# Optimization experiments

Measured on AMD Instinct MI355X. Metric: run time of the kernel, lower is better.

The kernel has to match this reference:

```python
import jax, jax.numpy as jnp
import numpy as np

B, T = 64, 2048
ENC_DIM, ATT_DIM, RNN_DIM, N_FILT, KSIZE, WIN = 512, 128, 1024, 32, 31, 32


def setup_inputs() -> dict:
    key = jax.random.key(0)
    ks = jax.random.split(key, 10)
    return {
        "attention_hidden_state": jax.random.normal(ks[0], (B, RNN_DIM), jnp.float32),
        "memory": jax.random.normal(ks[1], (B, T, ENC_DIM), jnp.float32),
        "processed_memory": jax.random.normal(ks[2], (B, T, ATT_DIM), jnp.float32),
        "attention_weights_cat": jax.random.uniform(ks[3], (B, 2, T), jnp.float32),
        "mask": jnp.zeros((B, T), jnp.bool_),
        "memory_lengths": jax.random.randint(ks[4], (B,), 0, T, jnp.int32),
        "current_pos": jax.random.uniform(ks[5], (B,), jnp.float32),
        "loc_conv_w": jax.random.normal(ks[6], (N_FILT, 2, KSIZE), jnp.float32) * 0.1,
        "loc_dense_w": jax.random.normal(ks[7], (ATT_DIM, N_FILT), jnp.float32) * 0.1,
        "query_w": jax.random.normal(ks[8], (ATT_DIM, RNN_DIM), jnp.float32) * 0.03,
        "v_w": jax.random.normal(ks[9], (1, ATT_DIM), jnp.float32) * 0.1,
        "pos_offset": jnp.zeros((1,), jnp.float32),
    }


def reference(attention_hidden_state, memory, processed_memory, attention_weights_cat,
              mask, memory_lengths, current_pos,
              loc_conv_w, loc_dense_w, query_w, v_w, pos_offset):
    Bn, Tn, _ = memory.shape
    pad = (KSIZE - 1) // 2
    # location conv: [B,2,T] -> [B,n_filters,T]
    conv = jax.lax.conv_general_dilated(
        attention_weights_cat, loc_conv_w, window_strides=(1,),
        padding=[(pad, pad)], dimension_numbers=("NCH", "OIH", "NCH"))
    # location dense + query projection + processed memory (fused add)
    processed = (jnp.einsum("bft,af->bta", conv, loc_dense_w)
                 + (attention_hidden_state @ query_w.T)[:, None, :]
                 + processed_memory)                      # [B,T,att_dim]
    alignment = jnp.tanh(processed) @ v_w[0]              # [B,T]
    # dynamic windowed mask around current_pos
    cp = current_pos + pos_offset[0]
    max_end = (memory_lengths - 1 - WIN).astype(cp.dtype)
    cp = jnp.minimum(jnp.maximum(cp, jnp.float32(WIN)), max_end)
    mask_start = jnp.round(jnp.maximum(cp - WIN, 0.0))
    mask_end = mask_start + 2 * WIN
    pos = jnp.arange(Tn, dtype=cp.dtype)
    pos_mask = (pos[None, :] >= mask_start[:, None]) & (pos[None, :] <= mask_end[:, None])
    full_mask = mask | ~pos_mask
    alignment = jnp.where(full_mask, jnp.float32(-1e9), alignment)
    attention_weights = jax.nn.softmax(alignment, axis=1)  # [B,T]
    attention_context = jnp.einsum("bt,btd->bd", attention_weights, memory)  # [B,enc_dim]
    new_pos = attention_weights @ jnp.arange(Tn, dtype=attention_weights.dtype)  # [B]
    return attention_context, attention_weights, new_pos
```

## Files before the change

### kernel.cpp

```cpp
#include <hip/hip_runtime.h>
#include <math.h>

#define Bn 64
#define Tn 2048
#define ENC 512
#define ATT 128
#define RNN 1024
#define NF 32
#define KS 31
#define WINR 32
#define WSZ 65
#define HALO 95
#define NTH 512

__global__ __launch_bounds__(NTH)
void attn_fused(
    const float* __restrict__ hidden,
    const float* __restrict__ memory,
    const float* __restrict__ pmem,
    const float* __restrict__ cat,
    const unsigned char* __restrict__ mask,
    const int*  __restrict__ mlen,
    const float* __restrict__ cpos,
    const float* __restrict__ convw,
    const float* __restrict__ densew,
    const float* __restrict__ qw,
    const float* __restrict__ vw,
    const float* __restrict__ posoff,
    float* __restrict__ out)
{
    __shared__ float s_hidden[RNN];
    __shared__ float s_part[NTH];
    __shared__ float s_qproj[ATT];
    __shared__ float s_ldw[ATT * 33];
    __shared__ float s_cw[NF * 2 * KS];
    __shared__ float s_cat[2 * HALO];
    __shared__ float s_conv[WSZ * NF];
    __shared__ float s_pm[WSZ * ATT];
    __shared__ unsigned char s_mk[WSZ];
    __shared__ float s_align[WSZ];
    __shared__ float s_w[WSZ];
    __shared__ float2 s_red[2 * (ENC / 2)];

    const int b = blockIdx.x;
    const int tid = threadIdx.x;

    float cp = cpos[b] + posoff[0];
    float mend = (float)(mlen[b] - 1 - WINR);
    cp = fminf(fmaxf(cp, (float)WINR), mend);
    int s = (int)rintf(fmaxf(cp - (float)WINR, 0.0f));
    if (s < 0) s = 0;
    if (s > Tn - WSZ) s = Tn - WSZ;

    for (int i = tid; i < RNN / 4; i += NTH)
        ((float4*)s_hidden)[i] = ((const float4*)(hidden + (size_t)b * RNN))[i];
    {
        const float4* pmw = (const float4*)(pmem + ((size_t)b * Tn + s) * ATT);
        for (int i = tid; i < WSZ * ATT / 4; i += NTH)
            ((float4*)s_pm)[i] = pmw[i];
    }
    for (int i = tid; i < ATT * NF; i += NTH) {
        int a = i >> 5, f = i & 31;
        s_ldw[a * 33 + f] = densew[i];
    }
    for (int i = tid; i < NF * 2 * KS; i += NTH) s_cw[i] = convw[i];
    for (int i = tid; i < 2 * HALO; i += NTH) {
        int cch = i / HALO, j = i - cch * HALO;
        int t = s - (KS - 1) / 2 + j;
        float v = 0.0f;
        if (t >= 0 && t < Tn) v = cat[((size_t)b * 2 + cch) * Tn + t];
        s_cat[cch * HALO + j] = v;
    }
    if (tid < WSZ) s_mk[tid] = mask[(size_t)b * Tn + s + tid];

    const int c = tid & 255;
    const int g = tid >> 8;
    float2 v[33];
    const float2* m2 = (const float2*)(memory + (size_t)b * Tn * ENC)
                       + (size_t)(s + g) * (ENC / 2) + c;
#pragma unroll
    for (int i = 0; i < 33; i++) {
        int j = g + 2 * i;
        if (j < WSZ) v[i] = m2[(size_t)(2 * i) * (ENC / 2)];
    }
    __syncthreads();

    {
        int a = tid & 127, q = tid >> 7;
        const float4* q4 = (const float4*)(qw + (size_t)a * RNN + q * 256);
        const float4* h4 = (const float4*)(s_hidden + q * 256);
        float acc = 0.0f;
#pragma unroll 8
        for (int i = 0; i < 64; i++) {
            float4 x = q4[i], h = h4[i];
            acc += x.x * h.x + x.y * h.y + x.z * h.z + x.w * h.w;
        }
        s_part[tid] = acc;
    }
    __syncthreads();
    if (tid < ATT)
        s_qproj[tid] = s_part[tid] + s_part[tid + 128] + s_part[tid + 256] + s_part[tid + 384];

    for (int i = tid; i < WSZ * NF; i += NTH) {
        int j = i >> 5, f = i & 31;
        const float* w0 = s_cw + f * 2 * KS;
        const float* c0 = s_cat + j;
        const float* c1 = s_cat + HALO + j;
        float acc = 0.0f;
#pragma unroll
        for (int k = 0; k < KS; k++) acc += c0[k] * w0[k] + c1[k] * w0[KS + k];
        s_conv[i] = acc;
    }
    __syncthreads();

    const int lane = tid & 63;
    const int wv = tid >> 6;
    const float va0 = vw[lane];
    const float va1 = vw[lane + 64];
    for (int j = wv; j < WSZ; j += 8) {
        const float* pmr = s_pm + j * ATT;
        const float* cv = s_conv + j * NF;
        const float* l0 = s_ldw + lane * 33;
        const float* l1 = s_ldw + (lane + 64) * 33;
        float x0 = s_qproj[lane] + pmr[lane];
        float x1 = s_qproj[lane + 64] + pmr[lane + 64];
#pragma unroll
        for (int f = 0; f < NF; f++) {
            float cc = cv[f];
            x0 += cc * l0[f];
            x1 += cc * l1[f];
        }
        float val = tanhf(x0) * va0 + tanhf(x1) * va1;
        for (int off = 32; off > 0; off >>= 1) val += __shfl_down(val, off);
        if (lane == 0) s_align[j] = s_mk[j] ? -1e9f : val;
    }
    __syncthreads();

    if (tid < WSZ) {
        float m = -1e30f;
        for (int j = 0; j < WSZ; j++) m = fmaxf(m, s_align[j]);
        float sum = 0.0f;
        for (int j = 0; j < WSZ; j++) sum += expf(s_align[j] - m);
        s_w[tid] = expf(s_align[tid] - m) / sum;
    }
    __syncthreads();

    if (tid == 0) {
        float np = 0.0f;
        for (int j = 0; j < WSZ; j++) np += s_w[j] * (float)(s + j);
        out[(size_t)Bn * ENC + (size_t)Bn * Tn + b] = np;
    }

    {
        float4* wout = (float4*)(out + (size_t)Bn * ENC + (size_t)b * Tn);
        for (int i = tid; i < Tn / 4; i += NTH) {
            float4 vv;
            float* vp = (float*)&vv;
#pragma unroll
            for (int q = 0; q < 4; q++) {
                int j = i * 4 + q - s;
                vp[q] = (j >= 0 && j < WSZ) ? s_w[j] : 0.0f;
            }
            wout[i] = vv;
        }
    }

    {
        float2 acc = make_float2(0.0f, 0.0f);
#pragma unroll
        for (int i = 0; i < 33; i++) {
            int j = g + 2 * i;
            if (j < WSZ) {
                float wj = s_w[j];
                acc.x += wj * v[i].x;
                acc.y += wj * v[i].y;
            }
        }
        s_red[g * (ENC / 2) + c] = acc;
    }
    __syncthreads();
    if (tid < ENC / 2) {
        float2 a = s_red[tid], bb = s_red[(ENC / 2) + tid];
        float2 r = make_float2(a.x + bb.x, a.y + bb.y);
        ((float2*)out)[(size_t)b * (ENC / 2) + tid] = r;
    }
}

extern "C" void kernel_launch(void* const* d_in, const int* in_sizes, int n_in,
                              void* d_out, int out_size, void* d_ws, size_t ws_size,
                              hipStream_t stream) {
    attn_fused<<<Bn, NTH, 0, stream>>>(
        (const float*)d_in[0],
        (const float*)d_in[1],
        (const float*)d_in[2],
        (const float*)d_in[3],
        (const unsigned char*)d_in[4],
        (const int*)d_in[5],
        (const float*)d_in[6],
        (const float*)d_in[7],
        (const float*)d_in[8],
        (const float*)d_in[9],
        (const float*)d_in[10],
        (const float*)d_in[11],
        (float*)d_out);
}
```

Measured before the change: 375.7 us.

## Warp-parallel query projection and softmax, pre-zero attention-weight row before window write

Reworks the query projection so each wavefront computes 16 output rows, with full-row float4 loads and a shuffle reduction. This removes the partial-sum shared array and one barrier. Replaces the serial per-thread softmax and new_pos loops with wavefront shuffle reductions. The attention-weight output row is zero-filled early, and only the 65-element window is written afterwards. Correctness depends on the zero fill being ordered before the window write within the same block, which the barriers provide.

```diff
diff --git a/kernel.cpp b/kernel.cpp
--- a/kernel.cpp
+++ b/kernel.cpp
@@ -30,7 +30,6 @@
     float* __restrict__ out)
 {
     __shared__ float s_hidden[RNN];
-    __shared__ float s_part[NTH];
     __shared__ float s_qproj[ATT];
     __shared__ float s_ldw[ATT * 33];
     __shared__ float s_cw[NF * 2 * KS];
@@ -44,6 +43,8 @@
 
     const int b = blockIdx.x;
     const int tid = threadIdx.x;
+    const int lane = tid & 63;
+    const int wv = tid >> 6;
 
     float cp = cpos[b] + posoff[0];
     float mend = (float)(mlen[b] - 1 - WINR);
@@ -73,6 +74,9 @@
     }
     if (tid < WSZ) s_mk[tid] = mask[(size_t)b * Tn + s + tid];
 
+    const float va0 = vw[lane];
+    const float va1 = vw[lane + 64];
+
     const int c = tid & 255;
     const int g = tid >> 8;
     float2 v[33];
@@ -83,23 +87,37 @@
         int j = g + 2 * i;
         if (j < WSZ) v[i] = m2[(size_t)(2 * i) * (ENC / 2)];
     }
-    __syncthreads();
-
-    {
-        int a = tid & 127, q = tid >> 7;
-        const float4* q4 = (const float4*)(qw + (size_t)a * RNN + q * 256);
-        const float4* h4 = (const float4*)(s_hidden + q * 256);
-        float acc = 0.0f;
-#pragma unroll 8
-        for (int i = 0; i < 64; i++) {
-            float4 x = q4[i], h = h4[i];
-            acc += x.x * h.x + x.y * h.y + x.z * h.z + x.w * h.w;
+
+    {
+        float4 z = make_float4(0.0f, 0.0f, 0.0f, 0.0f);
+        float4* wout = (float4*)(out + (size_t)Bn * ENC + (size_t)b * Tn);
+        for (int i = tid; i < Tn / 4; i += NTH) wout[i] = z;
+    }
+    __syncthreads();
+
+    {
+        const float4* h4 = (const float4*)s_hidden;
+        const float4 h0 = h4[lane];
+        const float4 h1 = h4[64 + lane];
+        const float4 h2 = h4[128 + lane];
+        const float4 h3 = h4[192 + lane];
+#pragma unroll 4
+        for (int r = 0; r < 16; r++) {
+            const int a = (wv << 4) + r;
+            const float4* qa = (const float4*)qw + (size_t)a * (RNN / 4);
+            float4 q0 = qa[lane];
+            float4 q1 = qa[64 + lane];
+            float4 q2 = qa[128 + lane];
+            float4 q3 = qa[192 + lane];
+            float acc = q0.x * h0.x + q0.y * h0.y + q0.z * h0.z + q0.w * h0.w
+                      + q1.x * h1.x + q1.y * h1.y + q1.z * h1.z + q1.w * h1.w
+                      + q2.x * h2.x + q2.y * h2.y + q2.z * h2.z + q2.w * h2.w
+                      + q3.x * h3.x + q3.y * h3.y + q3.z * h3.z + q3.w * h3.w;
+#pragma unroll
+            for (int off = 32; off > 0; off >>= 1) acc += __shfl_xor(acc, off);
+            if (lane == 0) s_qproj[a] = acc;
         }
-        s_part[tid] = acc;
-    }
-    __syncthreads();
-    if (tid < ATT)
-        s_qproj[tid] = s_part[tid] + s_part[tid + 128] + s_part[tid + 256] + s_part[tid + 384];
+    }
 
     for (int i = tid; i < WSZ * NF; i += NTH) {
         int j = i >> 5, f = i & 31;
@@ -113,10 +131,6 @@
     }
     __syncthreads();
 
-    const int lane = tid & 63;
-    const int wv = tid >> 6;
-    const float va0 = vw[lane];
-    const float va1 = vw[lane + 64];
     for (int j = wv; j < WSZ; j += 8) {
         const float* pmr = s_pm + j * ATT;
         const float* cv = s_conv + j * NF;
@@ -136,33 +150,31 @@
     }
     __syncthreads();
 
-    if (tid < WSZ) {
-        float m = -1e30f;
-        for (int j = 0; j < WSZ; j++) m = fmaxf(m, s_align[j]);
-        float sum = 0.0f;
-        for (int j = 0; j < WSZ; j++) sum += expf(s_align[j] - m);
-        s_w[tid] = expf(s_align[tid] - m) / sum;
-    }
-    __syncthreads();
-
-    if (tid == 0) {
-        float np = 0.0f;
-        for (int j = 0; j < WSZ; j++) np += s_w[j] * (float)(s + j);
-        out[(size_t)Bn * ENC + (size_t)Bn * Tn + b] = np;
-    }
-
-    {
-        float4* wout = (float4*)(out + (size_t)Bn * ENC + (size_t)b * Tn);
-        for (int i = tid; i < Tn / 4; i += NTH) {
-            float4 vv;
-            float* vp = (float*)&vv;
-#pragma unroll
-            for (int q = 0; q < 4; q++) {
-                int j = i * 4 + q - s;
-                vp[q] = (j >= 0 && j < WSZ) ? s_w[j] : 0.0f;
-            }
-            wout[i] = vv;
-        }
+    if (wv == 0) {
+        float a0 = s_align[lane];
+        float aex = (lane == 0) ? s_align[64] : -1e30f;
+        float m = fmaxf(a0, aex);
+#pragma unroll
+        for (int off = 32; off > 0; off >>= 1) m = fmaxf(m, __shfl_xor(m, off));
+        float e0 = expf(a0 - m);
+        float e64 = (lane == 0) ? expf(s_align[64] - m) : 0.0f;
+        float t = e0 + e64;
+#pragma unroll
+        for (int off = 32; off > 0; off >>= 1) t += __shfl_xor(t, off);
+        s_w[lane] = e0 / t;
+        if (lane == 0) s_w[64] = e64 / t;
+    }
+    __syncthreads();
+
+    if (tid < WSZ)
+        out[(size_t)Bn * ENC + (size_t)b * Tn + s + tid] = s_w[tid];
+
+    if (wv == 1) {
+        float np = s_w[lane] * (float)(s + lane);
+        if (lane == 0) np += s_w[64] * (float)(s + 64);
+#pragma unroll
+        for (int off = 32; off > 0; off >>= 1) np += __shfl_xor(np, off);
+        if (lane == 0) out[(size_t)Bn * ENC + (size_t)Bn * Tn + b] = np;
     }
 
     {
```

Result: faster. 367.3 us (-2.2%).
